# Kernel optimization log

Measured on AMD Instinct MI355X. Metric: run time of the kernel, lower is better.

Reference implementation:

```python
import jax, jax.numpy as jnp
import numpy as np

NEG = -1e9  # masked_fill value


def _forward(input1, input2, wg1, wg2):
    S, E = input1.shape[0], wg1.shape[0]
    k = E // 4                      # expert_group_size
    num_2nd = E // 4
    capacity = int(2 * ((S + num_2nd - 1) // num_2nd))  # training-mode capacity, cf=1.0

    # --- first-level group gating ---
    group_logits = input1 @ wg1.T                     # [S,E]
    group_gates = jax.nn.softmax(group_logits.at[:, 0].set(NEG), axis=1)
    _, top_idx = jax.lax.top_k(group_gates, k)        # [S,k]
    rows = jnp.arange(S)[:, None]
    group_mask = jnp.zeros((S, E), dtype=bool).at[rows, top_idx].set(True)

    # --- second-level logits, masked to the selected group ---
    logits = input2 @ wg2.T                           # [S,E]
    gates = jax.nn.softmax(jnp.where(group_mask, logits, NEG), axis=1)

    # --- htop1gating ---
    indices1 = jnp.argmax(gates, axis=1)              # [S]
    mask1 = jax.nn.one_hot(indices1, E, dtype=jnp.int32)   # [S,E]
    gates1_s = (gates * mask1).sum(axis=1)            # [S]
    locations1 = jnp.cumsum(mask1, axis=0) - 1        # [S,E]

    me = jnp.mean(gates, axis=0)
    ce = jnp.mean(mask1.astype(gates.dtype), axis=0)
    l_aux = jnp.sum(me * ce) / num_2nd * (E * E)

    mask1 = mask1 * (locations1 < capacity).astype(mask1.dtype)
    locations1_s = jnp.sum(locations1 * mask1, axis=1)          # [S]
    gates1 = gates1_s[:, None] * mask1.astype(gates1_s.dtype)   # [S,E]
    locations1_sc = jax.nn.one_hot(locations1_s, capacity, dtype=gates1.dtype)  # [S,C]
    combine = gates1[:, :, None] * locations1_sc[:, None, :]    # [S,E,C]
    dispatch = combine.astype(bool)
    return l_aux, combine, dispatch


def setup_inputs() -> dict:
    key = jax.random.key(0)
    k1, k2, k3, k4 = jax.random.split(key, 4)
    S, D, E = 4096, 1024, 64
    return {
        "input1": jax.random.normal(k1, (S, D), dtype=jnp.float32),
        "input2": jax.random.normal(k2, (S, D), dtype=jnp.float32),
        "wg1": jax.random.normal(k3, (E, D), dtype=jnp.float32) * 0.02,
        "wg2": jax.random.normal(k4, (E, D), dtype=jnp.float32) * 0.02,
    }


def reference(input1, input2, wg1, wg2):
    return _forward(input1, input2, wg1, wg2)
```

## Files before the change

### kernel.cpp

```cpp
#include <hip/hip_runtime.h>
#include <cstdint>
#include <cstddef>

#define S_ROWS 4096
#define DIM 1024
#define NE 64
#define CAP 512
#define NEGV -1e9f
#define NGEMM 128
#define NFILL 4096

typedef float v4f __attribute__((ext_vector_type(4)));

__global__ __launch_bounds__(256) void fusedA(const float* __restrict__ X1, const float* __restrict__ W1,
                                              const float* __restrict__ X2, const float* __restrict__ W2,
                                              int* __restrict__ eidx, float* __restrict__ gval,
                                              float* __restrict__ Gslot, int* __restrict__ Cslot,
                                              v4f* __restrict__ out4, long long n4,
                                              float* __restrict__ out, long long n) {
    const int bid = blockIdx.x;
    const int tid = threadIdx.x;

    __shared__ float As[32][68];
    __shared__ float Bs[64][68];
    __shared__ float Lg[2][32][68];
    __shared__ float sG[4][NE];
    __shared__ int   hist[NE];

    if (bid >= NGEMM) {
        long long i = (long long)(bid - NGEMM) * 256 + tid;
        const long long stride = (long long)(gridDim.x - NGEMM) * 256;
        v4f z = {0.f, 0.f, 0.f, 0.f};
        for (; i < n4; i += stride) __builtin_nontemporal_store(z, &out4[i]);
        if (bid == NGEMM && tid == 0)
            for (long long j = n4 * 4; j < n; ++j) out[j] = 0.f;
        return;
    }

    if (tid < NE) hist[tid] = 0;

    const int row0 = bid * 32;
    const int tx = tid & 15;
    const int ty = tid >> 4;

    #pragma unroll
    for (int m = 0; m < 2; ++m) {
        const float* __restrict__ X = m ? X2 : X1;
        const float* __restrict__ W = m ? W2 : W1;
        float acc[2][4] = {};
        for (int kk = 0; kk < DIM; kk += 64) {
            __syncthreads();
            #pragma unroll
            for (int p = 0; p < 2; ++p) {
                int r  = ty + p * 16;
                int c4 = tx * 4;
                float4 a = *(const float4*)&X[(size_t)(row0 + r) * DIM + kk + c4];
                *(float4*)&As[r][c4] = a;
            }
            #pragma unroll
            for (int p = 0; p < 4; ++p) {
                int e  = ty + p * 16;
                int c4 = tx * 4;
                float4 w = *(const float4*)&W[(size_t)e * DIM + kk + c4];
                Bs[c4 + 0][e] = w.x;
                Bs[c4 + 1][e] = w.y;
                Bs[c4 + 2][e] = w.z;
                Bs[c4 + 3][e] = w.w;
            }
            __syncthreads();
            #pragma unroll
            for (int k4 = 0; k4 < 64; k4 += 4) {
                float4 a[2], b[4];
                #pragma unroll
                for (int i = 0; i < 2; ++i) a[i] = *(float4*)&As[ty * 2 + i][k4];
                #pragma unroll
                for (int t = 0; t < 4; ++t) b[t] = *(float4*)&Bs[k4 + t][tx * 4];
                #pragma unroll
                for (int i = 0; i < 2; ++i) {
                    acc[i][0] += a[i].x * b[0].x + a[i].y * b[1].x + a[i].z * b[2].x + a[i].w * b[3].x;
                    acc[i][1] += a[i].x * b[0].y + a[i].y * b[1].y + a[i].z * b[2].y + a[i].w * b[3].y;
                    acc[i][2] += a[i].x * b[0].z + a[i].y * b[1].z + a[i].z * b[2].z + a[i].w * b[3].z;
                    acc[i][3] += a[i].x * b[0].w + a[i].y * b[1].w + a[i].z * b[2].w + a[i].w * b[3].w;
                }
            }
        }
        #pragma unroll
        for (int i = 0; i < 2; ++i)
            #pragma unroll
            for (int t = 0; t < 4; ++t)
                Lg[m][ty * 2 + i][tx * 4 + t] = acc[i][t];
    }
    __syncthreads();

    const int wid = tid >> 6, lane = tid & 63;
    float gacc = 0.f;
    #pragma unroll
    for (int i = 0; i < 8; ++i) {
        const int lr = wid * 8 + i;
        const int r  = row0 + lr;
        float l1 = Lg[0][lr][lane];
        if (lane == 0) l1 = NEGV;

        int cnt = 0;
        #pragma unroll
        for (int j = 0; j < 64; ++j) {
            float vj = __shfl(l1, j);
            cnt += (vj > l1 || (vj == l1 && j < lane));
        }
        const bool sel = cnt < 16;

        float l2 = Lg[1][lr][lane];
        float ml = sel ? l2 : NEGV;

        float mx = ml;
        #pragma unroll
        for (int o = 32; o; o >>= 1) mx = fmaxf(mx, __shfl_xor(mx, o));
        float ex = expf(ml - mx);
        float sum = ex;
        #pragma unroll
        for (int o = 32; o; o >>= 1) sum += __shfl_xor(sum, o);
        float g = ex / sum;
        gacc += g;

        float bg = g; int bi = lane;
        #pragma unroll
        for (int o = 32; o; o >>= 1) {
            float og = __shfl_xor(bg, o);
            int   oi = __shfl_xor(bi, o);
            if (og > bg || (og == bg && oi < bi)) { bg = og; bi = oi; }
        }
        if (lane == 0) {
            eidx[r] = bi;
            gval[r] = bg;
            atomicAdd(&hist[bi], 1);
        }
    }
    sG[wid][lane] = gacc;
    __syncthreads();
    if (tid < NE) {
        Gslot[bid * NE + tid] = sG[0][tid] + sG[1][tid] + sG[2][tid] + sG[3][tid];
        Cslot[bid * NE + tid] = hist[tid];
    }
}

__global__ __launch_bounds__(256) void finishB(const int* __restrict__ eidx, const float* __restrict__ gval,
                                               const float* __restrict__ Gslot, const int* __restrict__ Cslot,
                                               float* __restrict__ out) {
    const int s = blockIdx.x;
    if (s == S_ROWS) {
        if (threadIdx.x < NE) {
            const int e = threadIdx.x;
            float Ge = 0.f; int Ce = 0;
            for (int b = 0; b < NGEMM; ++b) {
                Ge += Gslot[b * NE + e];
                Ce += Cslot[b * NE + e];
            }
            float v = Ge * (float)Ce;
            #pragma unroll
            for (int o = 32; o; o >>= 1) v += __shfl_xor(v, o);
            if (e == 0) out[0] = v * (1.0f / 65536.0f);
        }
        return;
    }
    const int my = eidx[s];
    int cnt = 0;
    for (int j = threadIdx.x; j < s; j += 256) cnt += (eidx[j] == my);
    __shared__ int sc[4];
    #pragma unroll
    for (int o = 32; o; o >>= 1) cnt += __shfl_down(cnt, o);
    const int wid = threadIdx.x >> 6, lane = threadIdx.x & 63;
    if (lane == 0) sc[wid] = cnt;
    __syncthreads();
    if (threadIdx.x == 0) {
        int rank = sc[0] + sc[1] + sc[2] + sc[3];
        if (rank < CAP) {
            size_t base = 1 + (((size_t)s * NE + my) * CAP + (size_t)rank);
            out[base] = gval[s];
            out[base + (size_t)S_ROWS * NE * CAP] = 1.0f;
        }
    }
}

extern "C" void kernel_launch(void* const* d_in, const int* in_sizes, int n_in,
                              void* d_out, int out_size, void* d_ws, size_t ws_size,
                              hipStream_t stream) {
    const float* in1 = (const float*)d_in[0];
    const float* in2 = (const float*)d_in[1];
    const float* wg1 = (const float*)d_in[2];
    const float* wg2 = (const float*)d_in[3];
    float* out = (float*)d_out;

    int*   eidx  = (int*)d_ws;
    float* gv    = (float*)(eidx + S_ROWS);
    float* Gslot = gv + S_ROWS;
    int*   Cslot = (int*)(Gslot + NGEMM * NE);

    long long n  = (long long)out_size;
    long long n4 = n >> 2;

    fusedA<<<NGEMM + NFILL, 256, 0, stream>>>(in1, wg1, in2, wg2,
                                              eidx, gv, Gslot, Cslot,
                                              (v4f*)out, n4, out, n);
    finishB<<<S_ROWS + 1, 256, 0, stream>>>(eidx, gv, Gslot, Cslot, out);
}
```

Measured before the change: 1.075 ms.

## Compute capacity ranks in fused kernel via cross-block prefix of expert histograms

Drops the per-row scatter kernel, in which each of 4096 blocks rescanned all earlier expert indices to find its rank. The gating kernel now publishes its per-block expert histogram, sets a release flag, and waits for all lower-numbered blocks. It then computes each row's rank as the prefix sum of those histograms plus a local count, and the last gating block also computes l_aux. A small scatter kernel then writes the combine and dispatch entries. The flags are set to a magic value and never cleared, so on repeated calls the spin-wait can pass while it reads stale Cslot data, and the spin also assumes all 128 gating blocks are co-resident.

```diff
diff --git a/kernel.cpp b/kernel.cpp
--- a/kernel.cpp
+++ b/kernel.cpp
@@ -9,13 +9,29 @@
 #define NEGV -1e9f
 #define NGEMM 128
 #define NFILL 4096
+#define MAGIC 0x1F2E3D4C
 
 typedef float v4f __attribute__((ext_vector_type(4)));
+
+__device__ __forceinline__ int aloadi(const int* p) {
+    return __hip_atomic_load(p, __ATOMIC_RELAXED, __HIP_MEMORY_SCOPE_AGENT);
+}
+__device__ __forceinline__ float aloadf(const float* p) {
+    return __hip_atomic_load(p, __ATOMIC_RELAXED, __HIP_MEMORY_SCOPE_AGENT);
+}
+__device__ __forceinline__ void astorei(int* p, int v) {
+    __hip_atomic_store(p, v, __ATOMIC_RELAXED, __HIP_MEMORY_SCOPE_AGENT);
+}
+__device__ __forceinline__ void astoref(float* p, float v) {
+    __hip_atomic_store(p, v, __ATOMIC_RELAXED, __HIP_MEMORY_SCOPE_AGENT);
+}
 
 __global__ __launch_bounds__(256) void fusedA(const float* __restrict__ X1, const float* __restrict__ W1,
                                               const float* __restrict__ X2, const float* __restrict__ W2,
                                               int* __restrict__ eidx, float* __restrict__ gval,
+                                              int* __restrict__ rnk,
                                               float* __restrict__ Gslot, int* __restrict__ Cslot,
+                                              int* __restrict__ flags,
                                               v4f* __restrict__ out4, long long n4,
                                               float* __restrict__ out, long long n) {
     const int bid = blockIdx.x;
@@ -26,14 +42,19 @@
     __shared__ float Lg[2][32][68];
     __shared__ float sG[4][NE];
     __shared__ int   hist[NE];
+    __shared__ int   le[32];
+    __shared__ float lv[32];
 
     if (bid >= NGEMM) {
         long long i = (long long)(bid - NGEMM) * 256 + tid;
         const long long stride = (long long)(gridDim.x - NGEMM) * 256;
         v4f z = {0.f, 0.f, 0.f, 0.f};
-        for (; i < n4; i += stride) __builtin_nontemporal_store(z, &out4[i]);
-        if (bid == NGEMM && tid == 0)
+        for (; i < n4; i += stride)
+            if (i) __builtin_nontemporal_store(z, &out4[i]);
+        if (bid == NGEMM && tid == 0) {
+            out[1] = 0.f; out[2] = 0.f; out[3] = 0.f;
             for (long long j = n4 * 4; j < n; ++j) out[j] = 0.f;
+        }
         return;
     }
 
@@ -132,52 +153,56 @@
         if (lane == 0) {
             eidx[r] = bi;
             gval[r] = bg;
+            le[lr] = bi;
+            lv[lr] = bg;
             atomicAdd(&hist[bi], 1);
         }
     }
     sG[wid][lane] = gacc;
     __syncthreads();
+
     if (tid < NE) {
-        Gslot[bid * NE + tid] = sG[0][tid] + sG[1][tid] + sG[2][tid] + sG[3][tid];
-        Cslot[bid * NE + tid] = hist[tid];
-    }
-}
-
-__global__ __launch_bounds__(256) void finishB(const int* __restrict__ eidx, const float* __restrict__ gval,
-                                               const float* __restrict__ Gslot, const int* __restrict__ Cslot,
-                                               float* __restrict__ out) {
-    const int s = blockIdx.x;
-    if (s == S_ROWS) {
-        if (threadIdx.x < NE) {
-            const int e = threadIdx.x;
-            float Ge = 0.f; int Ce = 0;
-            for (int b = 0; b < NGEMM; ++b) {
-                Ge += Gslot[b * NE + e];
-                Ce += Cslot[b * NE + e];
-            }
-            float v = Ge * (float)Ce;
-            #pragma unroll
-            for (int o = 32; o; o >>= 1) v += __shfl_xor(v, o);
-            if (e == 0) out[0] = v * (1.0f / 65536.0f);
-        }
-        return;
-    }
-    const int my = eidx[s];
-    int cnt = 0;
-    for (int j = threadIdx.x; j < s; j += 256) cnt += (eidx[j] == my);
-    __shared__ int sc[4];
-    #pragma unroll
-    for (int o = 32; o; o >>= 1) cnt += __shfl_down(cnt, o);
-    const int wid = threadIdx.x >> 6, lane = threadIdx.x & 63;
-    if (lane == 0) sc[wid] = cnt;
+        astoref(&Gslot[bid * NE + tid], sG[0][tid] + sG[1][tid] + sG[2][tid] + sG[3][tid]);
+        astorei(&Cslot[bid * NE + tid], hist[tid]);
+    }
+    __threadfence();
+    if (tid == 0)
+        __hip_atomic_store(&flags[bid], MAGIC, __ATOMIC_RELEASE, __HIP_MEMORY_SCOPE_AGENT);
+
+    for (int b = tid; b < bid; b += 256)
+        while (__hip_atomic_load(&flags[b], __ATOMIC_ACQUIRE, __HIP_MEMORY_SCOPE_AGENT) != MAGIC)
+            __builtin_amdgcn_s_sleep(1);
     __syncthreads();
-    if (threadIdx.x == 0) {
-        int rank = sc[0] + sc[1] + sc[2] + sc[3];
-        if (rank < CAP) {
-            size_t base = 1 + (((size_t)s * NE + my) * CAP + (size_t)rank);
-            out[base] = gval[s];
-            out[base + (size_t)S_ROWS * NE * CAP] = 1.0f;
-        }
+
+    if (tid < 32) {
+        const int e = le[tid];
+        int p = 0;
+        for (int b = 0; b < bid; ++b) p += aloadi(&Cslot[b * NE + e]);
+        for (int j = 0; j < tid; ++j) p += (le[j] == e);
+        rnk[row0 + tid] = p;
+    }
+
+    if (bid == NGEMM - 1 && tid < NE) {
+        float Ge = 0.f; int Ce = 0;
+        for (int b = 0; b < NGEMM; ++b) {
+            Ge += aloadf(&Gslot[b * NE + tid]);
+            Ce += aloadi(&Cslot[b * NE + tid]);
+        }
+        float v = Ge * (float)Ce;
+        #pragma unroll
+        for (int o = 32; o; o >>= 1) v += __shfl_xor(v, o);
+        if (tid == 0) out[0] = v * (1.0f / 65536.0f);
+    }
+}
+
+__global__ __launch_bounds__(256) void scatterB(const int* __restrict__ eidx, const float* __restrict__ gval,
+                                                const int* __restrict__ rnk, float* __restrict__ out) {
+    const int s = blockIdx.x * 256 + threadIdx.x;
+    const int rank = rnk[s];
+    if (rank < CAP) {
+        const size_t base = 1 + (((size_t)s * NE + eidx[s]) * CAP + (size_t)rank);
+        out[base] = gval[s];
+        out[base + (size_t)S_ROWS * NE * CAP] = 1.0f;
     }
 }
 
@@ -192,14 +217,16 @@
 
     int*   eidx  = (int*)d_ws;
     float* gv    = (float*)(eidx + S_ROWS);
-    float* Gslot = gv + S_ROWS;
+    int*   rnk   = (int*)(gv + S_ROWS);
+    float* Gslot = (float*)(rnk + S_ROWS);
     int*   Cslot = (int*)(Gslot + NGEMM * NE);
+    int*   flags = Cslot + NGEMM * NE;
 
     long long n  = (long long)out_size;
     long long n4 = n >> 2;
 
     fusedA<<<NGEMM + NFILL, 256, 0, stream>>>(in1, wg1, in2, wg2,
-                                              eidx, gv, Gslot, Cslot,
+                                              eidx, gv, rnk, Gslot, Cslot, flags,
                                               (v4f*)out, n4, out, n);
-    finishB<<<S_ROWS + 1, 256, 0, stream>>>(eidx, gv, Gslot, Cslot, out);
-}
+    scatterB<<<S_ROWS / 256, 256, 0, stream>>>(eidx, gv, rnk, out);
+}
```

After: 1.099 ms. 1.02x slower.

## Compute capacity ranks from per-block expert histograms instead of quadratic scans

Applied to the files above, without the earlier changes.

The finishing kernel used to launch one block per token, and each block scanned every earlier token's expert index to find its rank, which is quadratic work. It now launches one 64-thread block per 32-token tile. Each block adds up the per-block expert histograms already produced by the GEMM kernel to get a prefix offset, then ranks its 32 tokens locally in shared memory. This removes most of the redundant global reads and the many launched blocks, at the cost of a serial prefix loop over up to 128 histogram slots per block.

```diff
diff --git a/kernel.cpp b/kernel.cpp
--- a/kernel.cpp
+++ b/kernel.cpp
@@ -143,38 +143,41 @@
     }
 }
 
-__global__ __launch_bounds__(256) void finishB(const int* __restrict__ eidx, const float* __restrict__ gval,
-                                               const float* __restrict__ Gslot, const int* __restrict__ Cslot,
-                                               float* __restrict__ out) {
-    const int s = blockIdx.x;
-    if (s == S_ROWS) {
-        if (threadIdx.x < NE) {
-            const int e = threadIdx.x;
-            float Ge = 0.f; int Ce = 0;
-            for (int b = 0; b < NGEMM; ++b) {
-                Ge += Gslot[b * NE + e];
-                Ce += Cslot[b * NE + e];
-            }
-            float v = Ge * (float)Ce;
-            #pragma unroll
-            for (int o = 32; o; o >>= 1) v += __shfl_xor(v, o);
-            if (e == 0) out[0] = v * (1.0f / 65536.0f);
-        }
+__global__ __launch_bounds__(64) void finishB(const int* __restrict__ eidx, const float* __restrict__ gval,
+                                              const float* __restrict__ Gslot, const int* __restrict__ Cslot,
+                                              float* __restrict__ out) {
+    const int bid = blockIdx.x;
+    const int tid = threadIdx.x;
+
+    if (bid == NGEMM) {
+        float Ge = 0.f; int Ce = 0;
+        for (int b = 0; b < NGEMM; ++b) {
+            Ge += Gslot[b * NE + tid];
+            Ce += Cslot[b * NE + tid];
+        }
+        float v = Ge * (float)Ce;
+        #pragma unroll
+        for (int o = 32; o; o >>= 1) v += __shfl_xor(v, o);
+        if (tid == 0) out[0] = v * (1.0f / 65536.0f);
         return;
     }
-    const int my = eidx[s];
-    int cnt = 0;
-    for (int j = threadIdx.x; j < s; j += 256) cnt += (eidx[j] == my);
-    __shared__ int sc[4];
-    #pragma unroll
-    for (int o = 32; o; o >>= 1) cnt += __shfl_down(cnt, o);
-    const int wid = threadIdx.x >> 6, lane = threadIdx.x & 63;
-    if (lane == 0) sc[wid] = cnt;
+
+    int pre = 0;
+    for (int b = 0; b < bid; ++b) pre += Cslot[b * NE + tid];
+
+    __shared__ int le[32];
+    __shared__ int pref[NE];
+    pref[tid] = pre;
+    if (tid < 32) le[tid] = eidx[bid * 32 + tid];
     __syncthreads();
-    if (threadIdx.x == 0) {
-        int rank = sc[0] + sc[1] + sc[2] + sc[3];
+
+    if (tid < 32) {
+        const int e = le[tid];
+        int rank = pref[e];
+        for (int j = 0; j < tid; ++j) rank += (le[j] == e);
         if (rank < CAP) {
-            size_t base = 1 + (((size_t)s * NE + my) * CAP + (size_t)rank);
+            const int s = bid * 32 + tid;
+            const size_t base = 1 + (((size_t)s * NE + e) * CAP + (size_t)rank);
             out[base] = gval[s];
             out[base + (size_t)S_ROWS * NE * CAP] = 1.0f;
         }
@@ -201,5 +204,5 @@
     fusedA<<<NGEMM + NFILL, 256, 0, stream>>>(in1, wg1, in2, wg2,
                                               eidx, gv, Gslot, Cslot,
                                               (v4f*)out, n4, out, n);
-    finishB<<<S_ROWS + 1, 256, 0, stream>>>(eidx, gv, Gslot, Cslot, out);
+    finishB<<<NGEMM + 1, 64, 0, stream>>>(eidx, gv, Gslot, Cslot, out);
 }
```

After: 1.085 ms. No clear change (+0.9%).
